# Optimization experiments

Measured on AMD Instinct MI355X. Metric: run time of the kernel, lower is better.

The kernel has to match this reference:

```python
import jax, jax.numpy as jnp
import numpy as np

N, P, D, FDIM, TFEAT = 65536, 6, 256, 8, 16
RAW_DIM = 4 + TFEAT  # 20
IN_DIM = 3 + FDIM + 3 + 3  # xyz + frame embedding + rigid xyz + viewdir = 17


def setup_inputs() -> dict:
    key = jax.random.key(0)
    ks = jax.random.split(key, 16)
    inp = {
        "tpts": jax.random.normal(ks[0], (N, P, 3), jnp.float32),
        "bigpts": jax.random.normal(ks[1], (N, P, 3), jnp.float32),
        "viewdir": jax.random.normal(ks[2], (N, P, 3), jnp.float32),
        "dists": jax.random.uniform(ks[3], (N,), jnp.float32),
        "part_dist": jax.random.uniform(ks[4], (1, N, P), jnp.float32),
        "frame_dim": jax.random.normal(ks[5], (FDIM,), jnp.float32),
        "W1": jax.random.normal(ks[6], (P, IN_DIM, D), jnp.float32) / np.sqrt(IN_DIM),
        "b1": jax.random.normal(ks[7], (P, D), jnp.float32) * 0.01,
        "W2": jax.random.normal(ks[8], (P, D, D), jnp.float32) / np.sqrt(D),
        "b2": jax.random.normal(ks[9], (P, D), jnp.float32) * 0.01,
        "W3": jax.random.normal(ks[10], (P, D, RAW_DIM), jnp.float32) / np.sqrt(D),
        "b3": jax.random.normal(ks[11], (P, RAW_DIM), jnp.float32) * 0.01,
        "Wocc": jax.random.normal(ks[12], (P, D, 1), jnp.float32) / np.sqrt(D),
        "bocc": jax.random.normal(ks[13], (P, 1), jnp.float32) * 0.01,
        "tflag": jax.random.randint(ks[14], (N, P), 0, 2).astype(bool),
    }
    return inp


def _part_mlps(tpts, bigpts, viewdir, frame_dim, W1, b1, W2, b2, W3, b3, Wocc, bocc):
    # Run all P part networks on all N points (batched per-part GEMMs).
    n = tpts.shape[0]
    frame = jnp.broadcast_to(frame_dim, (n, P, FDIM))
    x = jnp.concatenate([tpts, frame, bigpts, viewdir], axis=-1)  # (N,P,17)
    h = jax.nn.relu(jnp.einsum('npi,pid->npd', x, W1) + b1)
    h = jax.nn.relu(jnp.einsum('npd,pde->npe', h, W2) + b2)
    raw_p = jnp.einsum('npd,pdr->npr', h, W3) + b3               # (N,P,20)
    occ_p = jax.nn.sigmoid(jnp.einsum('npd,pdo->npo', h, Wocc) + bocc)  # (N,P,1)
    return raw_p, occ_p


def reference(tpts, bigpts, viewdir, dists, part_dist, frame_dim,
              W1, b1, W2, b2, W3, b3, Wocc, bocc, tflag):
    raw_p, occ_p = _part_mlps(tpts, bigpts, viewdir, frame_dim,
                              W1, b1, W2, b2, W3, b3, Wocc, bocc)
    # scatter-back equivalent: unflagged (point, part) slots stay zero
    flag = tflag[..., None].astype(raw_p.dtype)  # (N,P,1)
    raws = raw_p * flag                           # (N,P,20)
    occs = occ_p * flag                           # (N,P,1)
    # cfg.aggr == 'mean'
    raw = raws.mean(axis=1)                       # (N,20)
    occ = occs.mean(axis=1)                       # (N,1)
    tocc = occs[..., 0]                           # (N,P)
    return jnp.concatenate([raw, occ, tocc], axis=-1)  # (N, 20+1+P)
```

## Files before the change

### kernel.cpp

```cpp
#include <hip/hip_runtime.h>
#include <hip/hip_bf16.h>

using bf16 = __hip_bfloat16;
typedef __bf16 bf16x8 __attribute__((ext_vector_type(8)));
typedef __bf16 bf16x4v __attribute__((ext_vector_type(4)));
typedef float f32x4 __attribute__((ext_vector_type(4)));

#define MFMA16(a, b, c) __builtin_amdgcn_mfma_f32_16x16x32_bf16((a), (b), (c), 0, 0, 0)


__global__ void prep_kernel(const float* __restrict__ W1, const float* __restrict__ b1,
                            const float* __restrict__ W2, const float* __restrict__ W3,
                            const float* __restrict__ Wocc, __bf16* __restrict__ ws) {
  const int t = blockIdx.x * 256 + threadIdx.x;
  if (t < 49152) {
    const int p = t >> 13, r = t & 8191, n = r >> 5, c = r & 31;
    const float* src = W2 + p * 65536 + c * 8 * 256 + n;
    bf16x8 v;
#pragma unroll
    for (int j = 0; j < 8; ++j) v[j] = (__bf16)src[j * 256];
    *reinterpret_cast<bf16x8*>(&ws[49152 + p * 65536 + n * 256 + c * 8]) = v;
  } else if (t < 55296) {
    const int u = t - 49152;
    const int p = u >> 10, r = u & 1023, n = r >> 2, c = r & 3;
    bf16x8 v;
#pragma unroll
    for (int j = 0; j < 8; ++j) {
      const int k = c * 8 + j;
      float x = 0.f;
      if (k < 17) {
        const int ko = (k < 8) ? k + 3 : ((k < 11) ? k - 8 : k);
        x = W1[p * 4352 + ko * 256 + n];
      } else if (k == 17) {
        x = b1[p * 256 + n];
      }
      v[j] = (__bf16)x;
    }
    *reinterpret_cast<bf16x8*>(&ws[p * 8192 + n * 32 + c * 8]) = v;
  } else if (t < 61440) {
    const int u = t - 55296;
    const int p = u >> 10, r = u & 1023, row = r >> 5, c = r & 31;
    bf16x8 v;
#pragma unroll
    for (int j = 0; j < 8; ++j) {
      const int k = c * 8 + j;
      float x = 0.f;
      if (row < 20)       x = W3[p * 5120 + k * 20 + row];
      else if (row == 20) x = Wocc[p * 256 + k];
      v[j] = (__bf16)x;
    }
    *reinterpret_cast<bf16x8*>(&ws[442368 + p * 8192 + row * 256 + c * 8]) = v;
  }
}

__global__ __launch_bounds__(256, 2) void tpose_main(
    const float* __restrict__ tpts, const float* __restrict__ bigpts,
    const float* __restrict__ viewdir, const float* __restrict__ frame,
    const float* __restrict__ b2g, const float* __restrict__ b3g,
    const float* __restrict__ boccg, const int* __restrict__ tflag,
    const __bf16* __restrict__ ws, float* __restrict__ out) {
  const __bf16* __restrict__ W1t = ws;
  const __bf16* __restrict__ W2t = ws + 49152;
  const __bf16* __restrict__ W3t = ws + 442368;

  __shared__ __align__(16) __bf16 Xf[128 * 40];
  __shared__ __align__(16) __bf16 Hf[128 * 256];

  const int tid = threadIdx.x;
  const int w = tid >> 6;
  const int lane = tid & 63;
  const int lq = lane >> 4;
  const int ln = lane & 15;
  const int e = ln & 7;
  const int n0 = blockIdx.x * 128;

  if (tid < 128) {
    bf16x8 f8;
#pragma unroll
    for (int j = 0; j < 8; ++j) f8[j] = (__bf16)frame[j];
    *reinterpret_cast<bf16x8*>(&Xf[tid * 40]) = f8;
    bf16x8 z = {};
    z[1] = (__bf16)1.0f;
    *reinterpret_cast<bf16x8*>(&Xf[tid * 40 + 16]) = z;
    bf16x8 z2 = {};
    *reinterpret_cast<bf16x8*>(&Xf[tid * 40 + 24]) = z2;
  }

  const int role = tid & 3;
  const float* __restrict__ dynsrc =
      (role == 0) ? tpts : (role == 1) ? bigpts : viewdir;

  float pre[2][3];
  float flv[2];
#pragma unroll
  for (int pass = 0; pass < 2; ++pass) {
    const int pt = (tid >> 2) + pass * 64;
    const int base3 = (n0 + pt) * 18;
#pragma unroll
    for (int i = 0; i < 3; ++i) pre[pass][i] = dynsrc[base3 + i];
  }
#pragma unroll
  for (int s = 0; s < 2; ++s)
    flv[s] = (tflag[(n0 + w * 32 + s * 16 + ln) * 6] != 0) ? 1.f : 0.f;

  float psum0[2][4] = {{0.f, 0.f, 0.f, 0.f}, {0.f, 0.f, 0.f, 0.f}};
  float psum1[2][4] = {{0.f, 0.f, 0.f, 0.f}, {0.f, 0.f, 0.f, 0.f}};

  for (int p = 0; p < 6; ++p) {
    if (role < 3) {
#pragma unroll
      for (int pass = 0; pass < 2; ++pass) {
        const int pt = (tid >> 2) + pass * 64;
#pragma unroll
        for (int i = 0; i < 3; ++i)
          Xf[pt * 40 + 8 + role * 3 + i] = (__bf16)pre[pass][i];
      }
    }

    const int pn = (p < 5) ? p + 1 : 5;
    float fln[2];
#pragma unroll
    for (int pass = 0; pass < 2; ++pass) {
      const int pt = (tid >> 2) + pass * 64;
      const int base3 = ((n0 + pt) * 6 + pn) * 3;
#pragma unroll
      for (int i = 0; i < 3; ++i) pre[pass][i] = dynsrc[base3 + i];
    }
#pragma unroll
    for (int s = 0; s < 2; ++s)
      fln[s] = (tflag[(n0 + w * 32 + s * 16 + ln) * 6 + pn] != 0) ? 1.f : 0.f;

    __syncthreads();

    f32x4 acc[4][8];
#pragma unroll
    for (int mt = 0; mt < 4; ++mt)
#pragma unroll
      for (int nt = 0; nt < 8; ++nt) acc[mt][nt] = f32x4{0.f, 0.f, 0.f, 0.f};
    {
      bf16x8 aw[4];
#pragma unroll
      for (int mt = 0; mt < 4; ++mt)
        aw[mt] = *reinterpret_cast<const bf16x8*>(
            &W1t[p * 8192 + (w * 64 + mt * 16 + ln) * 32 + lq * 8]);
#pragma unroll
      for (int nt = 0; nt < 8; ++nt) {
        const bf16x8 xb =
            *reinterpret_cast<const bf16x8*>(&Xf[(nt * 16 + ln) * 40 + lq * 8]);
#pragma unroll
        for (int mt = 0; mt < 4; ++mt) acc[mt][nt] = MFMA16(aw[mt], xb, acc[mt][nt]);
      }
    }
#pragma unroll
    for (int mt = 0; mt < 4; ++mt) {
      const int c = w * 8 + mt * 2 + (lq >> 1);
      const int off = ((c ^ e) << 3) + (lq & 1) * 4;
#pragma unroll
      for (int nt = 0; nt < 8; ++nt) {
        bf16x4v hv;
#pragma unroll
        for (int r = 0; r < 4; ++r) hv[r] = (__bf16)fmaxf(acc[mt][nt][r], 0.f);
        *reinterpret_cast<bf16x4v*>(&Hf[(nt * 16 + ln) * 256 + off]) = hv;
      }
    }

    __syncthreads();

#pragma unroll
    for (int mt = 0; mt < 4; ++mt)
#pragma unroll
      for (int nt = 0; nt < 8; ++nt) acc[mt][nt] = f32x4{0.f, 0.f, 0.f, 0.f};
    const __bf16* __restrict__ w2p = W2t + p * 65536 + (w * 64 + ln) * 256 + lq * 8;
#pragma unroll
    for (int kk = 0; kk < 8; ++kk) {
      bf16x8 a2[4];
#pragma unroll
      for (int mt = 0; mt < 4; ++mt)
        a2[mt] = *reinterpret_cast<const bf16x8*>(w2p + mt * 4096 + kk * 32);
#pragma unroll
      for (int nt = 0; nt < 8; ++nt) {
        const bf16x8 hb = *reinterpret_cast<const bf16x8*>(
            &Hf[(nt * 16 + ln) * 256 + (((kk * 4 + lq) ^ e) << 3)]);
#pragma unroll
        for (int mt = 0; mt < 4; ++mt) acc[mt][nt] = MFMA16(a2[mt], hb, acc[mt][nt]);
      }
    }

    __syncthreads();

    {
      f32x4 b2v[4];
#pragma unroll
      for (int mt = 0; mt < 4; ++mt)
        b2v[mt] = *reinterpret_cast<const f32x4*>(
            &b2g[p * 256 + w * 64 + mt * 16 + lq * 4]);
#pragma unroll
      for (int mt = 0; mt < 4; ++mt) {
        const int c = w * 8 + mt * 2 + (lq >> 1);
        const int off = ((c ^ e) << 3) + (lq & 1) * 4;
#pragma unroll
        for (int nt = 0; nt < 8; ++nt) {
          bf16x4v hv;
#pragma unroll
          for (int r = 0; r < 4; ++r)
            hv[r] = (__bf16)fmaxf(acc[mt][nt][r] + b2v[mt][r], 0.f);
          *reinterpret_cast<bf16x4v*>(&Hf[(nt * 16 + ln) * 256 + off]) = hv;
        }
      }
    }

    __syncthreads();

    f32x4 acc3[2][2];
#pragma unroll
    for (int mt = 0; mt < 2; ++mt)
#pragma unroll
      for (int s = 0; s < 2; ++s) acc3[mt][s] = f32x4{0.f, 0.f, 0.f, 0.f};
    const __bf16* __restrict__ w3p = W3t + p * 8192 + ln * 256 + lq * 8;
#pragma unroll
    for (int kk = 0; kk < 8; ++kk) {
      bf16x8 a3[2];
#pragma unroll
      for (int mt = 0; mt < 2; ++mt)
        a3[mt] = *reinterpret_cast<const bf16x8*>(w3p + mt * 4096 + kk * 32);
#pragma unroll
      for (int s = 0; s < 2; ++s) {
        const bf16x8 hb = *reinterpret_cast<const bf16x8*>(
            &Hf[(w * 32 + s * 16 + ln) * 256 + (((kk * 4 + lq) ^ e) << 3)]);
#pragma unroll
        for (int mt = 0; mt < 2; ++mt) acc3[mt][s] = MFMA16(a3[mt], hb, acc3[mt][s]);
      }
    }

    {
      float b3v[2][4];
#pragma unroll
      for (int mt = 0; mt < 2; ++mt)
#pragma unroll
        for (int r = 0; r < 4; ++r) {
          const int d = mt * 16 + lq * 4 + r;
          float v = 0.f;
          if (d < 20)       v = b3g[p * 20 + d];
          else if (d == 20) v = boccg[p];
          b3v[mt][r] = v;
        }
#pragma unroll
      for (int s = 0; s < 2; ++s) {
        const int pt = n0 + w * 32 + s * 16 + ln;
#pragma unroll
        for (int r = 0; r < 4; ++r) psum0[s][r] += flv[s] * (acc3[0][s][r] + b3v[0][r]);
        if (lq == 0) {
#pragma unroll
          for (int r = 0; r < 4; ++r) psum1[s][r] += flv[s] * (acc3[1][s][r] + b3v[1][r]);
        } else if (lq == 1) {
          const float occ = 1.f / (1.f + __expf(-(acc3[1][s][0] + b3v[1][0])));
          out[pt * 27 + 21 + p] = flv[s] * occ;
          psum1[s][0] += flv[s] * occ;
        }
      }
    }

    flv[0] = fln[0];
    flv[1] = fln[1];
  }

  const float inv6 = 1.f / 6.f;
#pragma unroll
  for (int s = 0; s < 2; ++s) {
    const int pt = n0 + w * 32 + s * 16 + ln;
#pragma unroll
    for (int r = 0; r < 4; ++r) out[pt * 27 + lq * 4 + r] = psum0[s][r] * inv6;
    if (lq == 0) {
#pragma unroll
      for (int r = 0; r < 4; ++r) out[pt * 27 + 16 + r] = psum1[s][r] * inv6;
    } else if (lq == 1) {
      out[pt * 27 + 20] = psum1[s][0] * inv6;
    }
  }
}

extern "C" void kernel_launch(void* const* d_in, const int* in_sizes, int n_in,
                              void* d_out, int out_size, void* d_ws, size_t ws_size,
                              hipStream_t stream) {
  const float* tpts    = (const float*)d_in[0];
  const float* bigpts  = (const float*)d_in[1];
  const float* viewdir = (const float*)d_in[2];
  const float* frame   = (const float*)d_in[5];
  const float* W1      = (const float*)d_in[6];
  const float* b1      = (const float*)d_in[7];
  const float* W2      = (const float*)d_in[8];
  const float* b2      = (const float*)d_in[9];
  const float* W3      = (const float*)d_in[10];
  const float* b3      = (const float*)d_in[11];
  const float* Wocc    = (const float*)d_in[12];
  const float* bocc    = (const float*)d_in[13];
  const int*   tflag   = (const int*)d_in[14];
  __bf16* ws  = (__bf16*)d_ws;
  float*  out = (float*)d_out;

  prep_kernel<<<240, 256, 0, stream>>>(W1, b1, W2, W3, Wocc, ws);
  tpose_main<<<512, 256, 0, stream>>>(tpts, bigpts, viewdir, frame, b2, b3,
                                      bocc, tflag, ws, out);
}
```

Measured before the change: 203.5 us.

## Make each wave own its 32 points end-to-end, removing block barriers

Each wave now computes all 256 hidden units for its own 32 points instead of splitting the output dimension across waves over all 128 points. This removes the __syncthreads between layers and keeps the layer-2 activations in registers. Those activations are fed to layer 3 through ds_bpermute lane shuffles rather than a shared-memory round trip. In exchange every wave streams the full W2 and W3 from global/L2 (4x more weight traffic per block), and register pressure goes up.

```diff
diff --git a/kernel.cpp b/kernel.cpp
--- a/kernel.cpp
+++ b/kernel.cpp
@@ -2,8 +2,8 @@
 #include <hip/hip_bf16.h>
 
 using bf16 = __hip_bfloat16;
+using uint = unsigned int;
 typedef __bf16 bf16x8 __attribute__((ext_vector_type(8)));
-typedef __bf16 bf16x4v __attribute__((ext_vector_type(4)));
 typedef float f32x4 __attribute__((ext_vector_type(4)));
 
 #define MFMA16(a, b, c) __builtin_amdgcn_mfma_f32_16x16x32_bf16((a), (b), (c), 0, 0, 0)
@@ -51,6 +51,19 @@
     }
     *reinterpret_cast<bf16x8*>(&ws[442368 + p * 8192 + row * 256 + c * 8]) = v;
   }
+}
+
+__device__ __forceinline__ uint packrelu(float a, float b) {
+  __bf16 x = (__bf16)fmaxf(a, 0.f);
+  __bf16 y = (__bf16)fmaxf(b, 0.f);
+  return (uint)__builtin_bit_cast(unsigned short, x) |
+         ((uint)__builtin_bit_cast(unsigned short, y) << 16);
+}
+__device__ __forceinline__ uint pack2(float a, float b) {
+  __bf16 x = (__bf16)a;
+  __bf16 y = (__bf16)b;
+  return (uint)__builtin_bit_cast(unsigned short, x) |
+         ((uint)__builtin_bit_cast(unsigned short, y) << 16);
 }
 
 __global__ __launch_bounds__(256, 2) void tpose_main(
@@ -63,175 +76,128 @@
   const __bf16* __restrict__ W2t = ws + 49152;
   const __bf16* __restrict__ W3t = ws + 442368;
 
-  __shared__ __align__(16) __bf16 Xf[128 * 40];
-  __shared__ __align__(16) __bf16 Hf[128 * 256];
+  __shared__ __align__(16) __bf16 Xs[128 * 40];
+  __shared__ __align__(16) uint  H1s[16384];
 
   const int tid = threadIdx.x;
   const int w = tid >> 6;
   const int lane = tid & 63;
   const int lq = lane >> 4;
   const int ln = lane & 15;
-  const int e = ln & 7;
+  const int swz = (ln & 7) << 3;
   const int n0 = blockIdx.x * 128;
-
-  if (tid < 128) {
+  const int wpt0 = n0 + w * 32;
+
+  const int prow = lane >> 1;
+  const int role = lane & 1;
+  uint* xr = (uint*)&Xs[(w * 32 + prow) * 40];
+  if (role == 0) {
     bf16x8 f8;
 #pragma unroll
     for (int j = 0; j < 8; ++j) f8[j] = (__bf16)frame[j];
-    *reinterpret_cast<bf16x8*>(&Xf[tid * 40]) = f8;
-    bf16x8 z = {};
-    z[1] = (__bf16)1.0f;
-    *reinterpret_cast<bf16x8*>(&Xf[tid * 40 + 16]) = z;
-    bf16x8 z2 = {};
-    *reinterpret_cast<bf16x8*>(&Xf[tid * 40 + 24]) = z2;
-  }
-
-  const int role = tid & 3;
-  const float* __restrict__ dynsrc =
-      (role == 0) ? tpts : (role == 1) ? bigpts : viewdir;
-
-  float pre[2][3];
+    *reinterpret_cast<bf16x8*>(xr) = f8;
+  } else {
+#pragma unroll
+    for (int i = 9; i < 16; ++i) xr[i] = 0;
+  }
+
+  float pre[6];
+  {
+    const int b3i = (wpt0 + prow) * 18;
+    if (role == 0) {
+#pragma unroll
+      for (int i = 0; i < 3; ++i) { pre[i] = tpts[b3i + i]; pre[3 + i] = bigpts[b3i + i]; }
+    } else {
+#pragma unroll
+      for (int i = 0; i < 3; ++i) pre[i] = viewdir[b3i + i];
+    }
+  }
   float flv[2];
 #pragma unroll
-  for (int pass = 0; pass < 2; ++pass) {
-    const int pt = (tid >> 2) + pass * 64;
-    const int base3 = (n0 + pt) * 18;
-#pragma unroll
-    for (int i = 0; i < 3; ++i) pre[pass][i] = dynsrc[base3 + i];
-  }
-#pragma unroll
-  for (int s = 0; s < 2; ++s)
-    flv[s] = (tflag[(n0 + w * 32 + s * 16 + ln) * 6] != 0) ? 1.f : 0.f;
+  for (int nt = 0; nt < 2; ++nt)
+    flv[nt] = (tflag[(wpt0 + nt * 16 + ln) * 6] != 0) ? 1.f : 0.f;
 
   float psum0[2][4] = {{0.f, 0.f, 0.f, 0.f}, {0.f, 0.f, 0.f, 0.f}};
   float psum1[2][4] = {{0.f, 0.f, 0.f, 0.f}, {0.f, 0.f, 0.f, 0.f}};
 
+  uint* const h1w = &H1s[w * 4096];
+  const int idxA = ((2 * (lq & 1)) * 16 + ln) * 4;
+  const int idxB = idxA + 64;
+
   for (int p = 0; p < 6; ++p) {
-    if (role < 3) {
-#pragma unroll
-      for (int pass = 0; pass < 2; ++pass) {
-        const int pt = (tid >> 2) + pass * 64;
-#pragma unroll
-        for (int i = 0; i < 3; ++i)
-          Xf[pt * 40 + 8 + role * 3 + i] = (__bf16)pre[pass][i];
-      }
+    if (role == 0) {
+      xr[4] = pack2(pre[0], pre[1]);
+      xr[5] = pack2(pre[2], pre[3]);
+      xr[6] = pack2(pre[4], pre[5]);
+    } else {
+      xr[7] = pack2(pre[0], pre[1]);
+      xr[8] = pack2(pre[2], 1.0f);
     }
 
     const int pn = (p < 5) ? p + 1 : 5;
     float fln[2];
-#pragma unroll
-    for (int pass = 0; pass < 2; ++pass) {
-      const int pt = (tid >> 2) + pass * 64;
-      const int base3 = ((n0 + pt) * 6 + pn) * 3;
-#pragma unroll
-      for (int i = 0; i < 3; ++i) pre[pass][i] = dynsrc[base3 + i];
-    }
-#pragma unroll
-    for (int s = 0; s < 2; ++s)
-      fln[s] = (tflag[(n0 + w * 32 + s * 16 + ln) * 6 + pn] != 0) ? 1.f : 0.f;
-
-    __syncthreads();
-
-    f32x4 acc[4][8];
-#pragma unroll
-    for (int mt = 0; mt < 4; ++mt)
-#pragma unroll
-      for (int nt = 0; nt < 8; ++nt) acc[mt][nt] = f32x4{0.f, 0.f, 0.f, 0.f};
     {
-      bf16x8 aw[4];
-#pragma unroll
-      for (int mt = 0; mt < 4; ++mt)
-        aw[mt] = *reinterpret_cast<const bf16x8*>(
-            &W1t[p * 8192 + (w * 64 + mt * 16 + ln) * 32 + lq * 8]);
-#pragma unroll
-      for (int nt = 0; nt < 8; ++nt) {
-        const bf16x8 xb =
-            *reinterpret_cast<const bf16x8*>(&Xf[(nt * 16 + ln) * 40 + lq * 8]);
-#pragma unroll
-        for (int mt = 0; mt < 4; ++mt) acc[mt][nt] = MFMA16(aw[mt], xb, acc[mt][nt]);
-      }
-    }
-#pragma unroll
-    for (int mt = 0; mt < 4; ++mt) {
-      const int c = w * 8 + mt * 2 + (lq >> 1);
-      const int off = ((c ^ e) << 3) + (lq & 1) * 4;
-#pragma unroll
-      for (int nt = 0; nt < 8; ++nt) {
-        bf16x4v hv;
-#pragma unroll
-        for (int r = 0; r < 4; ++r) hv[r] = (__bf16)fmaxf(acc[mt][nt][r], 0.f);
-        *reinterpret_cast<bf16x4v*>(&Hf[(nt * 16 + ln) * 256 + off]) = hv;
-      }
-    }
-
-    __syncthreads();
-
-#pragma unroll
-    for (int mt = 0; mt < 4; ++mt)
-#pragma unroll
-      for (int nt = 0; nt < 8; ++nt) acc[mt][nt] = f32x4{0.f, 0.f, 0.f, 0.f};
-    const __bf16* __restrict__ w2p = W2t + p * 65536 + (w * 64 + ln) * 256 + lq * 8;
-#pragma unroll
-    for (int kk = 0; kk < 8; ++kk) {
-      bf16x8 a2[4];
-#pragma unroll
-      for (int mt = 0; mt < 4; ++mt)
-        a2[mt] = *reinterpret_cast<const bf16x8*>(w2p + mt * 4096 + kk * 32);
-#pragma unroll
-      for (int nt = 0; nt < 8; ++nt) {
-        const bf16x8 hb = *reinterpret_cast<const bf16x8*>(
-            &Hf[(nt * 16 + ln) * 256 + (((kk * 4 + lq) ^ e) << 3)]);
-#pragma unroll
-        for (int mt = 0; mt < 4; ++mt) acc[mt][nt] = MFMA16(a2[mt], hb, acc[mt][nt]);
-      }
-    }
-
-    __syncthreads();
-
-    {
-      f32x4 b2v[4];
-#pragma unroll
-      for (int mt = 0; mt < 4; ++mt)
-        b2v[mt] = *reinterpret_cast<const f32x4*>(
-            &b2g[p * 256 + w * 64 + mt * 16 + lq * 4]);
-#pragma unroll
-      for (int mt = 0; mt < 4; ++mt) {
-        const int c = w * 8 + mt * 2 + (lq >> 1);
-        const int off = ((c ^ e) << 3) + (lq & 1) * 4;
-#pragma unroll
-        for (int nt = 0; nt < 8; ++nt) {
-          bf16x4v hv;
-#pragma unroll
-          for (int r = 0; r < 4; ++r)
-            hv[r] = (__bf16)fmaxf(acc[mt][nt][r] + b2v[mt][r], 0.f);
-          *reinterpret_cast<bf16x4v*>(&Hf[(nt * 16 + ln) * 256 + off]) = hv;
-        }
-      }
-    }
-
-    __syncthreads();
+      const int b3i = ((wpt0 + prow) * 6 + pn) * 3;
+      if (role == 0) {
+#pragma unroll
+        for (int i = 0; i < 3; ++i) { pre[i] = tpts[b3i + i]; pre[3 + i] = bigpts[b3i + i]; }
+      } else {
+#pragma unroll
+        for (int i = 0; i < 3; ++i) pre[i] = viewdir[b3i + i];
+      }
+#pragma unroll
+      for (int nt = 0; nt < 2; ++nt)
+        fln[nt] = (tflag[(wpt0 + nt * 16 + ln) * 6 + pn] != 0) ? 1.f : 0.f;
+    }
+
+    const bf16x8 xb0 = *reinterpret_cast<const bf16x8*>(&Xs[(w * 32 + ln) * 40 + lq * 8]);
+    const bf16x8 xb1 = *reinterpret_cast<const bf16x8*>(&Xs[(w * 32 + 16 + ln) * 40 + lq * 8]);
+    const __bf16* __restrict__ w1p = W1t + p * 8192 + ln * 32 + lq * 8;
+#pragma unroll
+    for (int mt = 0; mt < 16; ++mt) {
+      const bf16x8 aw = *reinterpret_cast<const bf16x8*>(w1p + mt * 512);
+      f32x4 z = {0.f, 0.f, 0.f, 0.f};
+      const f32x4 h0 = MFMA16(aw, xb0, z);
+      const f32x4 h1 = MFMA16(aw, xb1, z);
+      const int cc = (mt * 8 + lq * 2) ^ swz;
+      uint2 s0, s1;
+      s0.x = packrelu(h0[0], h0[1]); s0.y = packrelu(h0[2], h0[3]);
+      s1.x = packrelu(h1[0], h1[1]); s1.y = packrelu(h1[2], h1[3]);
+      *reinterpret_cast<uint2*>(&h1w[ln * 128 + cc]) = s0;
+      *reinterpret_cast<uint2*>(&h1w[(16 + ln) * 128 + cc]) = s1;
+    }
+
+    bf16x8 hf[8][2];
+#pragma unroll
+    for (int kk = 0; kk < 8; ++kk)
+#pragma unroll
+      for (int nt = 0; nt < 2; ++nt)
+        hf[kk][nt] = *reinterpret_cast<const bf16x8*>(
+            &h1w[(nt * 16 + ln) * 128 + ((kk * 16 + lq * 4) ^ swz)]);
+
+    uint h2p[16][2][2];
+    const __bf16* __restrict__ w2p = W2t + p * 65536 + ln * 256 + lq * 8;
+#pragma unroll
+    for (int m2 = 0; m2 < 16; m2 += 2) {
+      const f32x4 bv0 = *reinterpret_cast<const f32x4*>(&b2g[p * 256 + m2 * 16 + lq * 4]);
+      const f32x4 bv1 = *reinterpret_cast<const f32x4*>(&b2g[p * 256 + m2 * 16 + 16 + lq * 4]);
+      f32x4 aA0 = bv0, aA1 = bv0, aB0 = bv1, aB1 = bv1;
+#pragma unroll
+      for (int kk = 0; kk < 8; ++kk) {
+        const bf16x8 a2A = *reinterpret_cast<const bf16x8*>(w2p + m2 * 4096 + kk * 32);
+        const bf16x8 a2B = *reinterpret_cast<const bf16x8*>(w2p + (m2 + 1) * 4096 + kk * 32);
+        aA0 = MFMA16(a2A, hf[kk][0], aA0);
+        aA1 = MFMA16(a2A, hf[kk][1], aA1);
+        aB0 = MFMA16(a2B, hf[kk][0], aB0);
+        aB1 = MFMA16(a2B, hf[kk][1], aB1);
+      }
+      h2p[m2][0][0] = packrelu(aA0[0], aA0[1]); h2p[m2][0][1] = packrelu(aA0[2], aA0[3]);
+      h2p[m2][1][0] = packrelu(aA1[0], aA1[1]); h2p[m2][1][1] = packrelu(aA1[2], aA1[3]);
+      h2p[m2 + 1][0][0] = packrelu(aB0[0], aB0[1]); h2p[m2 + 1][0][1] = packrelu(aB0[2], aB0[3]);
+      h2p[m2 + 1][1][0] = packrelu(aB1[0], aB1[1]); h2p[m2 + 1][1][1] = packrelu(aB1[2], aB1[3]);
+    }
 
     f32x4 acc3[2][2];
-#pragma unroll
-    for (int mt = 0; mt < 2; ++mt)
-#pragma unroll
-      for (int s = 0; s < 2; ++s) acc3[mt][s] = f32x4{0.f, 0.f, 0.f, 0.f};
-    const __bf16* __restrict__ w3p = W3t + p * 8192 + ln * 256 + lq * 8;
-#pragma unroll
-    for (int kk = 0; kk < 8; ++kk) {
-      bf16x8 a3[2];
-#pragma unroll
-      for (int mt = 0; mt < 2; ++mt)
-        a3[mt] = *reinterpret_cast<const bf16x8*>(w3p + mt * 4096 + kk * 32);
-#pragma unroll
-      for (int s = 0; s < 2; ++s) {
-        const bf16x8 hb = *reinterpret_cast<const bf16x8*>(
-            &Hf[(w * 32 + s * 16 + ln) * 256 + (((kk * 4 + lq) ^ e) << 3)]);
-#pragma unroll
-        for (int mt = 0; mt < 2; ++mt) acc3[mt][s] = MFMA16(a3[mt], hb, acc3[mt][s]);
-      }
-    }
-
     {
       float b3v[2][4];
 #pragma unroll
@@ -245,18 +211,47 @@
           b3v[mt][r] = v;
         }
 #pragma unroll
-      for (int s = 0; s < 2; ++s) {
-        const int pt = n0 + w * 32 + s * 16 + ln;
-#pragma unroll
-        for (int r = 0; r < 4; ++r) psum0[s][r] += flv[s] * (acc3[0][s][r] + b3v[0][r]);
-        if (lq == 0) {
-#pragma unroll
-          for (int r = 0; r < 4; ++r) psum1[s][r] += flv[s] * (acc3[1][s][r] + b3v[1][r]);
-        } else if (lq == 1) {
-          const float occ = 1.f / (1.f + __expf(-(acc3[1][s][0] + b3v[1][0])));
-          out[pt * 27 + 21 + p] = flv[s] * occ;
-          psum1[s][0] += flv[s] * occ;
+      for (int mt = 0; mt < 2; ++mt)
+#pragma unroll
+        for (int nt = 0; nt < 2; ++nt)
+#pragma unroll
+          for (int r = 0; r < 4; ++r) acc3[mt][nt][r] = b3v[mt][r];
+    }
+    const __bf16* __restrict__ w3p = W3t + p * 8192 + ln * 256 + lq * 8;
+#pragma unroll
+    for (int kk = 0; kk < 8; ++kk) {
+      const bf16x8 a30 = *reinterpret_cast<const bf16x8*>(w3p + kk * 32);
+      const bf16x8 a31 = *reinterpret_cast<const bf16x8*>(w3p + 4096 + kk * 32);
+#pragma unroll
+      for (int nt = 0; nt < 2; ++nt) {
+        uint bw[4];
+#pragma unroll
+        for (int j = 0; j < 4; ++j) {
+          const int idx = (j < 2) ? idxA : idxB;
+          const int u = j & 1;
+          const uint lo = (uint)__builtin_amdgcn_ds_bpermute(idx, (int)h2p[2 * kk][nt][u]);
+          const uint hi = (uint)__builtin_amdgcn_ds_bpermute(idx, (int)h2p[2 * kk + 1][nt][u]);
+          bw[j] = (lq < 2) ? lo : hi;
         }
+        union { uint u4[4]; bf16x8 v; } cv;
+        cv.u4[0] = bw[0]; cv.u4[1] = bw[1]; cv.u4[2] = bw[2]; cv.u4[3] = bw[3];
+        acc3[0][nt] = MFMA16(a30, cv.v, acc3[0][nt]);
+        acc3[1][nt] = MFMA16(a31, cv.v, acc3[1][nt]);
+      }
+    }
+
+#pragma unroll
+    for (int nt = 0; nt < 2; ++nt) {
+      const int pt = wpt0 + nt * 16 + ln;
+#pragma unroll
+      for (int r = 0; r < 4; ++r) psum0[nt][r] += flv[nt] * acc3[0][nt][r];
+      if (lq == 0) {
+#pragma unroll
+        for (int r = 0; r < 4; ++r) psum1[nt][r] += flv[nt] * acc3[1][nt][r];
+      } else if (lq == 1) {
+        const float occ = 1.f / (1.f + __expf(-acc3[1][nt][0]));
+        out[pt * 27 + 21 + p] = flv[nt] * occ;
+        psum1[nt][0] += flv[nt] * occ;
       }
     }
 
@@ -266,15 +261,15 @@
 
   const float inv6 = 1.f / 6.f;
 #pragma unroll
-  for (int s = 0; s < 2; ++s) {
-    const int pt = n0 + w * 32 + s * 16 + ln;
-#pragma unroll
-    for (int r = 0; r < 4; ++r) out[pt * 27 + lq * 4 + r] = psum0[s][r] * inv6;
+  for (int nt = 0; nt < 2; ++nt) {
+    const int pt = wpt0 + nt * 16 + ln;
+#pragma unroll
+    for (int r = 0; r < 4; ++r) out[pt * 27 + lq * 4 + r] = psum0[nt][r] * inv6;
     if (lq == 0) {
 #pragma unroll
-      for (int r = 0; r < 4; ++r) out[pt * 27 + 16 + r] = psum1[s][r] * inv6;
+      for (int r = 0; r < 4; ++r) out[pt * 27 + 16 + r] = psum1[nt][r] * inv6;
     } else if (lq == 1) {
-      out[pt * 27 + 20] = psum1[s][0] * inv6;
+      out[pt * 27 + 20] = psum1[nt][0] * inv6;
     }
   }
 }
```

Result: slower. 329.1 us (+61.7%).
